# Optimization experiments

Hardware: AMD Instinct MI355X
Metric: run time of the kernel (lower is better)

Reference implementation:

```python
import jax, jax.numpy as jnp
import numpy as np

B, T, C, H = 4, 1024, 2048, 16
D = C // H  # head dim = 128
ALPHA_Q, BETA_Q = -128, 127


def _quant_params(w):
    # symmetric range per tensor, as in get_symmetric_range/get_tensor_quantization_parameters
    beta = float(np.abs(w).max())
    alpha = -beta
    s = (beta - alpha) / (BETA_Q - ALPHA_Q)
    z = int((beta * ALPHA_Q - alpha * BETA_Q) / (beta - alpha))
    return s, z


def _quantize(w, s, z):
    return np.clip(np.round(w / s + z), ALPHA_Q, BETA_Q).astype(np.int8)


def setup_inputs() -> dict:
    key = jax.random.key(0)
    x = jax.random.normal(key, (B, T, C), dtype=jnp.float32)
    rng = np.random.default_rng(0)
    # fp32 master weights (GPT init scale), then quantize per-tensor symmetric int8
    params = {
        'w_attn': rng.normal(0.0, 0.02, (3 * C, C)).astype(np.float32),
        'b_attn': rng.normal(0.0, 0.02, (3 * C,)).astype(np.float32),
        'w_proj': rng.normal(0.0, 0.02, (C, C)).astype(np.float32),
        'b_proj': rng.normal(0.0, 0.02, (C,)).astype(np.float32),
    }
    out = {'x': x}
    for name, arr in params.items():
        s, z = _quant_params(arr)
        out[name + '_q'] = jnp.asarray(_quantize(arr, s, z))
        out['s_' + name] = jnp.float32(s)
        out['z_' + name] = z  # python int, zero-point constant
    return out


def _dequant(wq, s, z):
    # dequantize_tensor: s * (int8 -> int32 - z) -> float32
    return s * (wq.astype(jnp.int32) - z).astype(jnp.float32)


def reference(x, w_attn_q, s_w_attn, z_w_attn, b_attn_q, s_b_attn, z_b_attn,
              w_proj_q, s_w_proj, z_w_proj, b_proj_q, s_b_proj, z_b_proj):
    wa = _dequant(w_attn_q, s_w_attn, z_w_attn)   # [3C, C]
    ba = _dequant(b_attn_q, s_b_attn, z_b_attn)   # [3C]
    wp = _dequant(w_proj_q, s_w_proj, z_w_proj)   # [C, C]
    bp = _dequant(b_proj_q, s_b_proj, z_b_proj)   # [C]

    qkv = jnp.einsum('btc,oc->bto', x, wa) + ba   # [B,T,3C]
    q, k, v = jnp.split(qkv, 3, axis=-1)
    # [B,T,C] -> [B,H,T,D]
    q = q.reshape(B, T, H, D).transpose(0, 2, 1, 3)
    k = k.reshape(B, T, H, D).transpose(0, 2, 1, 3)
    v = v.reshape(B, T, H, D).transpose(0, 2, 1, 3)

    scale = 1.0 / jnp.sqrt(jnp.float32(D))
    scores = jnp.einsum('bhqd,bhkd->bhqk', q, k) * scale  # [B,H,T,T]
    causal = jnp.tril(jnp.ones((T, T), dtype=bool))
    scores = jnp.where(causal, scores, jnp.finfo(scores.dtype).min)
    att = jax.nn.softmax(scores, axis=-1)
    y = jnp.einsum('bhqk,bhkd->bhqd', att, v)      # [B,H,T,D]
    y = y.transpose(0, 2, 1, 3).reshape(B, T, C)

    return jnp.einsum('btc,oc->bto', y, wp) + bp   # [B,T,C]
```

## Files before the change

### kernel.cpp

```cpp
#include <hip/hip_runtime.h>
#include <stdint.h>
#include <math.h>

typedef unsigned short u16;
typedef __attribute__((ext_vector_type(4))) float f32x4;
typedef __attribute__((ext_vector_type(4))) int i32x4;
typedef __attribute__((ext_vector_type(8))) short bf16x8;

__device__ __forceinline__ u16 f2bf(float f) {
  uint32_t u = __float_as_uint(f);
  u += 0x7FFFu + ((u >> 16) & 1u);
  return (u16)(u >> 16);
}

__device__ __forceinline__ void async16(const void* g, void* l) {
  __builtin_amdgcn_global_load_lds(
      (const __attribute__((address_space(1))) void*)g,
      (__attribute__((address_space(3))) void*)l, 16, 0, 0);
}

__global__ void absmax_x(const float4* __restrict__ x, float* __restrict__ amax_arr, int n4) {
  __shared__ float red[4];
  int i = blockIdx.x * 256 + threadIdx.x;
  float m = 0.f;
  for (; i < n4; i += gridDim.x * 256) {
    float4 v = x[i];
    m = fmaxf(m, fmaxf(fmaxf(fabsf(v.x), fabsf(v.y)), fmaxf(fabsf(v.z), fabsf(v.w))));
  }
#pragma unroll
  for (int s = 1; s < 64; s <<= 1) m = fmaxf(m, __shfl_xor(m, s));
  if ((threadIdx.x & 63) == 0) red[threadIdx.x >> 6] = m;
  __syncthreads();
  if (threadIdx.x == 0)
    amax_arr[blockIdx.x] = fmaxf(fmaxf(red[0], red[1]), fmaxf(red[2], red[3]));
}

__global__ void prep_fused(
    const float4* __restrict__ x, char4* __restrict__ xq,
    const int4* __restrict__ waq, char4* __restrict__ wa8, const int* __restrict__ z_wa,
    const int4* __restrict__ wpq, ushort4* __restrict__ wp_bf,
    const float* __restrict__ s_wp, const int* __restrict__ z_wp,
    const float* __restrict__ amax_arr, float* __restrict__ amax_final) {
  const int bid = blockIdx.x;
  const int tid = threadIdx.x;
  if (bid < 8192) {
    const int lane = tid & 63;
    float m = 0.f;
#pragma unroll
    for (int k = 0; k < 4; ++k) {
      float4 a = ((const float4*)amax_arr)[lane * 4 + k];
      m = fmaxf(m, fmaxf(fmaxf(a.x, a.y), fmaxf(a.z, a.w)));
    }
#pragma unroll
    for (int s = 1; s < 64; s <<= 1) m = fmaxf(m, __shfl_xor(m, s));
    if (bid == 0 && tid == 0) amax_final[0] = m;
    const float inv = 127.0f / m;
    const int i = bid * 256 + tid;
    float4 v = x[i];
    char4 r;
    r.x = (char)__float2int_rn(v.x * inv);
    r.y = (char)__float2int_rn(v.y * inv);
    r.z = (char)__float2int_rn(v.z * inv);
    r.w = (char)__float2int_rn(v.w * inv);
    xq[i] = r;
  } else if (bid < 20480) {
    const int zv = z_wa[0];
    const int i = (bid - 8192) * 256 + tid;
    int4 v = waq[i];
    char4 r;
    r.x = (char)(v.x - zv); r.y = (char)(v.y - zv);
    r.z = (char)(v.z - zv); r.w = (char)(v.w - zv);
    wa8[i] = r;
  } else {
    const float sv = s_wp[0];
    const int zv = z_wp[0];
    const int i = (bid - 20480) * 256 + tid;
    int4 v = wpq[i];
    ushort4 r;
    r.x = f2bf(sv * (float)(v.x - zv));
    r.y = f2bf(sv * (float)(v.y - zv));
    r.z = f2bf(sv * (float)(v.z - zv));
    r.w = f2bf(sv * (float)(v.w - zv));
    wp_bf[i] = r;
  }
}

__global__ __launch_bounds__(256, 2) void gemm_i8_qkv(
    const char* __restrict__ A, const char* __restrict__ B, int K,
    const float* __restrict__ sw, const float* __restrict__ amaxf,
    const int* __restrict__ bq, const float* __restrict__ bs, const int* __restrict__ bz,
    u16* __restrict__ qb, u16* __restrict__ kb, u16* __restrict__ vT) {
  __shared__ uint8_t sA[16384];
  __shared__ uint8_t sB[16384];
  const int tid = threadIdx.x;
  const int wave = tid >> 6, lane = tid & 63;
  const int quad = lane >> 4, l16 = lane & 15;
  const int wm = wave >> 1, wn = wave & 1;
  const int Mb = blockIdx.y << 7, Nb = blockIdx.x << 7;

  const char* ag[4];
  const char* bg[4];
  int lo[4];
#pragma unroll
  for (int i = 0; i < 4; ++i) {
    int row = wave * 32 + i * 8 + (lane >> 3);
    int c = (lane & 7) ^ (row & 7);
    ag[i] = A + (size_t)(Mb + row) * K + c * 16;
    bg[i] = B + (size_t)(Nb + row) * K + c * 16;
    lo[i] = wave * 4096 + i * 1024 + lane * 16;
  }

  i32x4 acc[4][4] = {};

  for (int kk = 0; kk < K; kk += 128) {
    __syncthreads();
#pragma unroll
    for (int i = 0; i < 4; ++i) {
      async16(ag[i] + kk, sA + lo[i]);
      async16(bg[i] + kk, sB + lo[i]);
    }
    __syncthreads();
#pragma unroll
    for (int ks = 0; ks < 2; ++ks) {
      i32x4 af[4], bfr[4];
#pragma unroll
      for (int t = 0; t < 4; ++t) {
        int m = wm * 64 + t * 16 + l16;
        af[t] = *(const i32x4*)(sA + m * 128 + ((((ks << 2) + quad) ^ (m & 7)) << 4));
        int n = wn * 64 + t * 16 + l16;
        bfr[t] = *(const i32x4*)(sB + n * 128 + ((((ks << 2) + quad) ^ (n & 7)) << 4));
      }
#pragma unroll
      for (int mt = 0; mt < 4; ++mt)
#pragma unroll
        for (int nt = 0; nt < 4; ++nt)
          acc[mt][nt] = __builtin_amdgcn_mfma_i32_16x16x64_i8(af[mt], bfr[nt], acc[mt][nt], 0, 0, 0);
    }
  }

  const float sv = sw[0] * (amaxf[0] / 127.0f);
  const float sbv = bs[0];
  const int zbv = bz[0];
#pragma unroll
  for (int nt = 0; nt < 4; ++nt) {
    const int o = Nb + wn * 64 + nt * 16 + l16;
    const float bias = sbv * (float)(bq[o] - zbv);
    const int which = o >> 11;
    const int cc = o & 2047;
    const int h = cc >> 7, d = cc & 127;
#pragma unroll
    for (int mt = 0; mt < 4; ++mt) {
      const int m0 = Mb + wm * 64 + mt * 16 + quad * 4;
      const int bi = m0 >> 10, t0 = m0 & 1023;
      const size_t bhx = (size_t)bi * 16 + h;
      if (which == 2) {
        ushort4 pv;
        pv.x = f2bf((float)acc[mt][nt][0] * sv + bias);
        pv.y = f2bf((float)acc[mt][nt][1] * sv + bias);
        pv.z = f2bf((float)acc[mt][nt][2] * sv + bias);
        pv.w = f2bf((float)acc[mt][nt][3] * sv + bias);
        *(ushort4*)(vT + (bhx * 128 + d) * 1024 + t0) = pv;
      } else {
        u16* dst = (which == 0 ? qb : kb) + (bhx * 1024 + t0) * 128 + d;
#pragma unroll
        for (int r = 0; r < 4; ++r) dst[r * 128] = f2bf((float)acc[mt][nt][r] * sv + bias);
      }
    }
  }
}

__global__ __launch_bounds__(256, 2) void gemm_bt_out(
    const u16* __restrict__ A, const u16* __restrict__ B, int K, int N,
    const int* __restrict__ bq, const float* __restrict__ bs, const int* __restrict__ bz,
    float* __restrict__ out) {
  __shared__ uint8_t sA[16384];
  __shared__ uint8_t sB[16384];
  const int tid = threadIdx.x;
  const int wave = tid >> 6, lane = tid & 63;
  const int quad = lane >> 4, l16 = lane & 15;
  const int wm = wave >> 1, wn = wave & 1;
  const int Mb = blockIdx.y << 7, Nb = blockIdx.x << 7;

  const u16* ag[4];
  const u16* bg[4];
  int lo[4];
#pragma unroll
  for (int i = 0; i < 4; ++i) {
    int row = wave * 32 + i * 8 + (lane >> 3);
    int c = (lane & 7) ^ (row & 7);
    ag[i] = A + (size_t)(Mb + row) * K + c * 8;
    bg[i] = B + (size_t)(Nb + row) * K + c * 8;
    lo[i] = wave * 4096 + i * 1024 + lane * 16;
  }

  f32x4 acc[4][4] = {};

  for (int kk = 0; kk < K; kk += 64) {
    __syncthreads();
#pragma unroll
    for (int i = 0; i < 4; ++i) {
      async16(ag[i] + kk, sA + lo[i]);
      async16(bg[i] + kk, sB + lo[i]);
    }
    __syncthreads();
#pragma unroll
    for (int ks = 0; ks < 2; ++ks) {
      bf16x8 af[4], bfr[4];
#pragma unroll
      for (int t = 0; t < 4; ++t) {
        int m = wm * 64 + t * 16 + l16;
        af[t] = *(const bf16x8*)(sA + m * 128 + ((((ks << 2) + quad) ^ (m & 7)) << 4));
        int n = wn * 64 + t * 16 + l16;
        bfr[t] = *(const bf16x8*)(sB + n * 128 + ((((ks << 2) + quad) ^ (n & 7)) << 4));
      }
#pragma unroll
      for (int mt = 0; mt < 4; ++mt)
#pragma unroll
        for (int nt = 0; nt < 4; ++nt)
          acc[mt][nt] = __builtin_amdgcn_mfma_f32_16x16x32_bf16(af[mt], bfr[nt], acc[mt][nt], 0, 0, 0);
    }
  }

  const float sbv = bs[0];
  const int zbv = bz[0];
#pragma unroll
  for (int nt = 0; nt < 4; ++nt) {
    const int o = Nb + wn * 64 + nt * 16 + l16;
    const float bias = sbv * (float)(bq[o] - zbv);
#pragma unroll
    for (int mt = 0; mt < 4; ++mt) {
      const int m0 = Mb + wm * 64 + mt * 16 + quad * 4;
#pragma unroll
      for (int r = 0; r < 4; ++r)
        out[(size_t)(m0 + r) * N + o] = acc[mt][nt][r] + bias;
    }
  }
}

__global__ __launch_bounds__(256, 2) void attn_fwd(
    const u16* __restrict__ qg, const u16* __restrict__ kg,
    const u16* __restrict__ vg, u16* __restrict__ yb) {
  __shared__ uint8_t smem[81920];
  uint8_t* sVb = smem + 32768;
  uint8_t* sP = smem + 65536;
  const int tid = threadIdx.x;
  const int wave = tid >> 6, lane = tid & 63;
  const int quad = lane >> 4, l16 = lane & 15;
  const int bh = blockIdx.x;
  const int y = blockIdx.y;
  const int qi = (y < 4) ? (7 - y) : (y - 4);
  const int qbase = qi << 7;
  const size_t base = (size_t)bh << 17;
  const u16* Q = qg + base;
  const u16* Kp = kg + base;
  const u16* Vp = vg + base;

#pragma unroll
  for (int i = 0; i < 8; ++i) {
    int off = wave * 8192 + i * 1024;
    int row = (off >> 8) + quad;
    int c = l16 ^ (row & 15);
    async16(Q + (size_t)(qbase + row) * 128 + c * 8, smem + off + lane * 16);
  }
  __syncthreads();
  bf16x8 qf[2][4];
#pragma unroll
  for (int mi = 0; mi < 2; ++mi)
#pragma unroll
    for (int ks = 0; ks < 4; ++ks) {
      int m = wave * 32 + mi * 16 + l16;
      qf[mi][ks] = *(const bf16x8*)(smem + m * 256 + ((((ks << 2) + quad) ^ (m & 15)) << 4));
    }
  asm volatile("s_waitcnt lgkmcnt(0)" ::: "memory");
  __builtin_amdgcn_sched_barrier(0);
  __builtin_amdgcn_s_barrier();

#define STAGEKV(TB, SL) do {                                                  \
    _Pragma("unroll")                                                         \
    for (int i_ = 0; i_ < 4; ++i_) {                                          \
      int off_ = wave * 4096 + i_ * 1024;                                     \
      int rowk_ = (off_ >> 8) + quad;                                         \
      int ck_ = l16 ^ (rowk_ & 15);                                           \
      async16(Kp + (size_t)((TB) + rowk_) * 128 + ck_ * 8,                    \
              smem + (SL) * 16384 + off_ + lane * 16);                        \
      int rowd_ = (off_ >> 7) + (lane >> 3);                                  \
      int cv_ = (lane & 7) ^ (rowd_ & 7);                                     \
      async16(Vp + (size_t)rowd_ * 1024 + (TB) + cv_ * 8,                     \
              sVb + (SL) * 16384 + off_ + lane * 16);                         \
    }                                                                         \
  } while (0)

  f32x4 accO[2][8] = {};
  float lacc[2][4] = {};

  const float scale = 0.088388347648318447f;
  const int jmax = 2 * qi + 1;

  STAGEKV(0, 0);

  for (int j = 0; j <= jmax; ++j) {
    const int tb = j << 6;
    const int jn = (j + 1 <= jmax) ? j + 1 : jmax;
    STAGEKV(jn << 6, (j + 1) & 1);
    asm volatile("s_waitcnt vmcnt(8)" ::: "memory");
    __builtin_amdgcn_s_barrier();
    const uint8_t* sK = smem + (j & 1) * 16384;
    const uint8_t* sV = sVb + (j & 1) * 16384;

    f32x4 sc[2][4] = {};
#pragma unroll
    for (int ks = 0; ks < 4; ++ks) {
      bf16x8 kf[4];
#pragma unroll
      for (int ni = 0; ni < 4; ++ni) {
        int n = ni * 16 + l16;
        kf[ni] = *(const bf16x8*)(sK + n * 256 + ((((ks << 2) + quad) ^ (n & 15)) << 4));
      }
#pragma unroll
      for (int mi = 0; mi < 2; ++mi)
#pragma unroll
        for (int ni = 0; ni < 4; ++ni)
          sc[mi][ni] = __builtin_amdgcn_mfma_f32_16x16x32_bf16(qf[mi][ks], kf[ni], sc[mi][ni], 0, 0, 0);
    }

    const bool needmask = (tb + 63) > qbase;
#pragma unroll
    for (int mi = 0; mi < 2; ++mi) {
      const int row0 = qbase + wave * 32 + mi * 16 + quad * 4;
#pragma unroll
      for (int ni = 0; ni < 4; ++ni) {
        const int col = tb + ni * 16 + l16;
#pragma unroll
        for (int r = 0; r < 4; ++r) {
          float s = sc[mi][ni][r] * scale;
          if (needmask && col > row0 + r) s = -INFINITY;
          float p = __expf(s);
          sc[mi][ni][r] = p;
          lacc[mi][r] += p;
        }
      }
    }

#pragma unroll
    for (int mi = 0; mi < 2; ++mi)
#pragma unroll
      for (int ni = 0; ni < 4; ++ni)
#pragma unroll
        for (int r = 0; r < 4; ++r) {
          int qr = wave * 32 + mi * 16 + quad * 4 + r;
          int kc = ni * 16 + l16;
          *(u16*)(sP + qr * 128 + (((kc >> 3) ^ (qr & 7)) << 4) + (kc & 7) * 2) =
              f2bf(sc[mi][ni][r]);
        }

#pragma unroll
    for (int ks = 0; ks < 2; ++ks) {
      bf16x8 pf[2], vf[8];
#pragma unroll
      for (int mi = 0; mi < 2; ++mi) {
        int m = wave * 32 + mi * 16 + l16;
        pf[mi] = *(const bf16x8*)(sP + m * 128 + ((((ks << 2) + quad) ^ (m & 7)) << 4));
      }
#pragma unroll
      for (int ni = 0; ni < 8; ++ni) {
        int n = ni * 16 + l16;
        vf[ni] = *(const bf16x8*)(sV + n * 128 + ((((ks << 2) + quad) ^ (n & 7)) << 4));
      }
#pragma unroll
      for (int mi = 0; mi < 2; ++mi)
#pragma unroll
        for (int ni = 0; ni < 8; ++ni)
          accO[mi][ni] = __builtin_amdgcn_mfma_f32_16x16x32_bf16(pf[mi], vf[ni], accO[mi][ni], 0, 0, 0);
    }
    __builtin_amdgcn_s_barrier();
  }
  asm volatile("s_waitcnt vmcnt(0)" ::: "memory");

  const int b = bh >> 4, h = bh & 15;
#pragma unroll
  for (int mi = 0; mi < 2; ++mi) {
    float inv[4];
#pragma unroll
    for (int r = 0; r < 4; ++r) {
      float l = lacc[mi][r];
#pragma unroll
      for (int x = 1; x < 16; x <<= 1) l += __shfl_xor(l, x);
      inv[r] = 1.0f / l;
    }
#pragma unroll
    for (int ni = 0; ni < 8; ++ni)
#pragma unroll
      for (int r = 0; r < 4; ++r) {
        int row = qbase + wave * 32 + mi * 16 + quad * 4 + r;
        int col = (h << 7) + ni * 16 + l16;
        yb[((size_t)(b * 1024 + row) << 11) + col] = f2bf(accO[mi][ni][r] * inv[r]);
      }
  }
#undef STAGEKV
}

extern "C" void kernel_launch(void* const* d_in, const int* in_sizes, int n_in,
                              void* d_out, int out_size, void* d_ws, size_t ws_size,
                              hipStream_t stream) {
  const float* x = (const float*)d_in[0];
  const int* waq = (const int*)d_in[1];
  const float* s_wa = (const float*)d_in[2];
  const int* z_wa = (const int*)d_in[3];
  const int* baq = (const int*)d_in[4];
  const float* s_ba = (const float*)d_in[5];
  const int* z_ba = (const int*)d_in[6];
  const int* wpq = (const int*)d_in[7];
  const float* s_wp = (const float*)d_in[8];
  const int* z_wp = (const int*)d_in[9];
  const int* bpq = (const int*)d_in[10];
  const float* s_bp = (const float*)d_in[11];
  const int* z_bp = (const int*)d_in[12];

  char* ws = (char*)d_ws;
  char* xq    = ws + 0;
  char* wa8   = ws + 8388608;
  u16* wp_bf  = (u16*)(ws + 20971520);
  u16* qb     = (u16*)(ws + 29360128);
  u16* kb     = (u16*)(ws + 46137344);
  u16* vT     = (u16*)(ws + 62914560);
  u16* yb     = (u16*)(ws + 79691776);
  float* amax_arr   = (float*)(ws + 96468992);
  float* amax_final = (float*)(ws + 96473088);

  absmax_x<<<1024, 256, 0, stream>>>((const float4*)x, amax_arr, 2097152);
  prep_fused<<<24576, 256, 0, stream>>>(
      (const float4*)x, (char4*)xq,
      (const int4*)waq, (char4*)wa8, z_wa,
      (const int4*)wpq, (ushort4*)wp_bf, s_wp, z_wp,
      amax_arr, amax_final);

  gemm_i8_qkv<<<dim3(48, 32), 256, 0, stream>>>(xq, wa8, 2048, s_wa, amax_final,
                                                baq, s_ba, z_ba, qb, kb, vT);

  attn_fwd<<<dim3(64, 8), 256, 0, stream>>>(qb, kb, vT, yb);

  gemm_bt_out<<<dim3(16, 32), 256, 0, stream>>>(yb, wp_bf, 2048, 2048,
                                                bpq, s_bp, z_bp, (float*)d_out);
}
```

Before: 289.6 us.

## Merge all stages into one persistent kernel with software grid barriers

```diff
diff --git a/kernel.cpp b/kernel.cpp
--- a/kernel.cpp
+++ b/kernel.cpp
@@ -19,261 +19,215 @@
       (__attribute__((address_space(3))) void*)l, 16, 0, 0);
 }
 
-__global__ void absmax_x(const float4* __restrict__ x, float* __restrict__ amax_arr, int n4) {
-  __shared__ float red[4];
-  int i = blockIdx.x * 256 + threadIdx.x;
-  float m = 0.f;
-  for (; i < n4; i += gridDim.x * 256) {
-    float4 v = x[i];
-    m = fmaxf(m, fmaxf(fmaxf(fabsf(v.x), fabsf(v.y)), fmaxf(fabsf(v.z), fabsf(v.w))));
-  }
-#pragma unroll
-  for (int s = 1; s < 64; s <<= 1) m = fmaxf(m, __shfl_xor(m, s));
-  if ((threadIdx.x & 63) == 0) red[threadIdx.x >> 6] = m;
+__device__ __forceinline__ void gbar(unsigned* cnt, unsigned* gen) {
   __syncthreads();
-  if (threadIdx.x == 0)
-    amax_arr[blockIdx.x] = fmaxf(fmaxf(red[0], red[1]), fmaxf(red[2], red[3]));
+  if (threadIdx.x == 0) {
+    unsigned g = __hip_atomic_load(gen, __ATOMIC_RELAXED, __HIP_MEMORY_SCOPE_AGENT);
+    unsigned prev = __hip_atomic_fetch_add(cnt, 1u, __ATOMIC_ACQ_REL, __HIP_MEMORY_SCOPE_AGENT);
+    if (prev == 511u) {
+      __hip_atomic_store(cnt, 0u, __ATOMIC_RELAXED, __HIP_MEMORY_SCOPE_AGENT);
+      __hip_atomic_store(gen, (g + 1u) & 3u, __ATOMIC_RELEASE, __HIP_MEMORY_SCOPE_AGENT);
+    } else {
+      unsigned t = 0;
+      while (__hip_atomic_load(gen, __ATOMIC_RELAXED, __HIP_MEMORY_SCOPE_AGENT) == g) {
+        __builtin_amdgcn_s_sleep(4);
+        if (++t > 2000000u) break;
+      }
+      __builtin_amdgcn_fence(__ATOMIC_ACQUIRE, "agent");
+    }
+  }
+  __syncthreads();
 }
 
-__global__ void prep_fused(
-    const float4* __restrict__ x, char4* __restrict__ xq,
-    const int4* __restrict__ waq, char4* __restrict__ wa8, const int* __restrict__ z_wa,
-    const int4* __restrict__ wpq, ushort4* __restrict__ wp_bf,
-    const float* __restrict__ s_wp, const int* __restrict__ z_wp,
-    const float* __restrict__ amax_arr, float* __restrict__ amax_final) {
-  const int bid = blockIdx.x;
-  const int tid = threadIdx.x;
-  if (bid < 8192) {
-    const int lane = tid & 63;
-    float m = 0.f;
-#pragma unroll
-    for (int k = 0; k < 4; ++k) {
-      float4 a = ((const float4*)amax_arr)[lane * 4 + k];
-      m = fmaxf(m, fmaxf(fmaxf(a.x, a.y), fmaxf(a.z, a.w)));
-    }
-#pragma unroll
-    for (int s = 1; s < 64; s <<= 1) m = fmaxf(m, __shfl_xor(m, s));
-    if (bid == 0 && tid == 0) amax_final[0] = m;
-    const float inv = 127.0f / m;
-    const int i = bid * 256 + tid;
-    float4 v = x[i];
-    char4 r;
-    r.x = (char)__float2int_rn(v.x * inv);
-    r.y = (char)__float2int_rn(v.y * inv);
-    r.z = (char)__float2int_rn(v.z * inv);
-    r.w = (char)__float2int_rn(v.w * inv);
-    xq[i] = r;
-  } else if (bid < 20480) {
-    const int zv = z_wa[0];
-    const int i = (bid - 8192) * 256 + tid;
-    int4 v = waq[i];
-    char4 r;
-    r.x = (char)(v.x - zv); r.y = (char)(v.y - zv);
-    r.z = (char)(v.z - zv); r.w = (char)(v.w - zv);
-    wa8[i] = r;
-  } else {
-    const float sv = s_wp[0];
-    const int zv = z_wp[0];
-    const int i = (bid - 20480) * 256 + tid;
-    int4 v = wpq[i];
-    ushort4 r;
-    r.x = f2bf(sv * (float)(v.x - zv));
-    r.y = f2bf(sv * (float)(v.y - zv));
-    r.z = f2bf(sv * (float)(v.z - zv));
-    r.w = f2bf(sv * (float)(v.w - zv));
-    wp_bf[i] = r;
-  }
-}
-
-__global__ __launch_bounds__(256, 2) void gemm_i8_qkv(
-    const char* __restrict__ A, const char* __restrict__ B, int K,
-    const float* __restrict__ sw, const float* __restrict__ amaxf,
-    const int* __restrict__ bq, const float* __restrict__ bs, const int* __restrict__ bz,
-    u16* __restrict__ qb, u16* __restrict__ kb, u16* __restrict__ vT) {
-  __shared__ uint8_t sA[16384];
-  __shared__ uint8_t sB[16384];
+__global__ __launch_bounds__(256, 2) void mega(
+    const float4* __restrict__ x,
+    const int4* __restrict__ waq, const int* __restrict__ z_wa,
+    const float* __restrict__ s_wa,
+    const int* __restrict__ baq, const float* __restrict__ s_ba, const int* __restrict__ z_ba,
+    const int4* __restrict__ wpq, const float* __restrict__ s_wp, const int* __restrict__ z_wp,
+    const int* __restrict__ bpq, const float* __restrict__ s_bp, const int* __restrict__ z_bp,
+    char* __restrict__ xq, char* __restrict__ wa8, u16* __restrict__ wp_bf,
+    u16* __restrict__ qb, u16* __restrict__ kb, u16* __restrict__ vT,
+    u16* __restrict__ yb, float* __restrict__ partial,
+    unsigned* __restrict__ bcnt, unsigned* __restrict__ bgen,
+    float* __restrict__ out) {
+  __shared__ uint8_t smem[81920];
+  const int rb = blockIdx.x;
   const int tid = threadIdx.x;
   const int wave = tid >> 6, lane = tid & 63;
   const int quad = lane >> 4, l16 = lane & 15;
-  const int wm = wave >> 1, wn = wave & 1;
-  const int Mb = blockIdx.y << 7, Nb = blockIdx.x << 7;
-
-  const char* ag[4];
-  const char* bg[4];
-  int lo[4];
-#pragma unroll
-  for (int i = 0; i < 4; ++i) {
-    int row = wave * 32 + i * 8 + (lane >> 3);
-    int c = (lane & 7) ^ (row & 7);
-    ag[i] = A + (size_t)(Mb + row) * K + c * 16;
-    bg[i] = B + (size_t)(Nb + row) * K + c * 16;
-    lo[i] = wave * 4096 + i * 1024 + lane * 16;
-  }
-
-  i32x4 acc[4][4] = {};
-
-  for (int kk = 0; kk < K; kk += 128) {
+
+  {
+    float m = 0.f;
+    for (int i = rb * 256 + tid; i < 2097152; i += 131072) {
+      float4 v = x[i];
+      m = fmaxf(m, fmaxf(fmaxf(fabsf(v.x), fabsf(v.y)), fmaxf(fabsf(v.z), fabsf(v.w))));
+    }
+#pragma unroll
+    for (int s = 1; s < 64; s <<= 1) m = fmaxf(m, __shfl_xor(m, s));
+    float* red = (float*)smem;
+    if (lane == 0) red[wave] = m;
     __syncthreads();
-#pragma unroll
-    for (int i = 0; i < 4; ++i) {
-      async16(ag[i] + kk, sA + lo[i]);
-      async16(bg[i] + kk, sB + lo[i]);
+    if (tid == 0)
+      partial[rb] = fmaxf(fmaxf(red[0], red[1]), fmaxf(red[2], red[3]));
+  }
+  gbar(bcnt, bgen);
+
+  float amax_val;
+  {
+    float m = 0.f;
+#pragma unroll
+    for (int k = 0; k < 2; ++k) {
+      float4 a = ((const float4*)partial)[lane * 2 + k];
+      m = fmaxf(m, fmaxf(fmaxf(a.x, a.y), fmaxf(a.z, a.w)));
+    }
+#pragma unroll
+    for (int s = 1; s < 64; s <<= 1) m = fmaxf(m, __shfl_xor(m, s));
+    amax_val = m;
+    const float inv = 127.0f / m;
+    for (int i = rb * 256 + tid; i < 2097152; i += 131072) {
+      float4 v = x[i];
+      char4 r;
+      r.x = (char)__float2int_rn(v.x * inv);
+      r.y = (char)__float2int_rn(v.y * inv);
+      r.z = (char)__float2int_rn(v.z * inv);
+      r.w = (char)__float2int_rn(v.w * inv);
+      ((char4*)xq)[i] = r;
+    }
+    const int zv = z_wa[0];
+    for (int i = rb * 256 + tid; i < 3145728; i += 131072) {
+      int4 v = waq[i];
+      char4 r;
+      r.x = (char)(v.x - zv); r.y = (char)(v.y - zv);
+      r.z = (char)(v.z - zv); r.w = (char)(v.w - zv);
+      ((char4*)wa8)[i] = r;
+    }
+    const float svp = s_wp[0];
+    const int zvp = z_wp[0];
+    for (int i = rb * 256 + tid; i < 1048576; i += 131072) {
+      int4 v = wpq[i];
+      ushort4 r;
+      r.x = f2bf(svp * (float)(v.x - zvp));
+      r.y = f2bf(svp * (float)(v.y - zvp));
+      r.z = f2bf(svp * (float)(v.z - zvp));
+      r.w = f2bf(svp * (float)(v.w - zvp));
+      ((ushort4*)wp_bf)[i] = r;
+    }
+  }
+  gbar(bcnt, bgen);
+
+  {
+    uint8_t* sA = smem;
+    uint8_t* sB = smem + 16384;
+    const char* A = xq;
+    const char* B = wa8;
+    const int wm = wave >> 1, wn = wave & 1;
+    const float sv = s_wa[0] * (amax_val / 127.0f);
+    const float sbv = s_ba[0];
+    const int zbv = z_ba[0];
+#pragma unroll 1
+    for (int vt = 0; vt < 3; ++vt) {
+      const int vb = rb + (vt << 9);
+      const int Mb = (vb / 48) << 7, Nb = (vb % 48) << 7;
+      const char* ag[4];
+      const char* bg[4];
+      int lo[4];
+#pragma unroll
+      for (int i = 0; i < 4; ++i) {
+        int row = wave * 32 + i * 8 + (lane >> 3);
+        int c = (lane & 7) ^ (row & 7);
+        ag[i] = A + (size_t)(Mb + row) * 2048 + c * 16;
+        bg[i] = B + (size_t)(Nb + row) * 2048 + c * 16;
+        lo[i] = wave * 4096 + i * 1024 + lane * 16;
+      }
+      i32x4 acc[4][4] = {};
+#pragma unroll 1
+      for (int kk = 0; kk < 2048; kk += 128) {
+        __syncthreads();
+#pragma unroll
+        for (int i = 0; i < 4; ++i) {
+          async16(ag[i] + kk, sA + lo[i]);
+          async16(bg[i] + kk, sB + lo[i]);
+        }
+        __syncthreads();
+#pragma unroll
+        for (int ks = 0; ks < 2; ++ks) {
+          i32x4 af[4], bfr[4];
+#pragma unroll
+          for (int t = 0; t < 4; ++t) {
+            int m = wm * 64 + t * 16 + l16;
+            af[t] = *(const i32x4*)(sA + m * 128 + ((((ks << 2) + quad) ^ (m & 7)) << 4));
+            int n = wn * 64 + t * 16 + l16;
+            bfr[t] = *(const i32x4*)(sB + n * 128 + ((((ks << 2) + quad) ^ (n & 7)) << 4));
+          }
+#pragma unroll
+          for (int mt = 0; mt < 4; ++mt)
+#pragma unroll
+            for (int nt = 0; nt < 4; ++nt)
+              acc[mt][nt] = __builtin_amdgcn_mfma_i32_16x16x64_i8(af[mt], bfr[nt], acc[mt][nt], 0, 0, 0);
+        }
+      }
+#pragma unroll
+      for (int nt = 0; nt < 4; ++nt) {
+        const int o = Nb + wn * 64 + nt * 16 + l16;
+        const float bias = sbv * (float)(baq[o] - zbv);
+        const int which = o >> 11;
+        const int cc = o & 2047;
+        const int h = cc >> 7, d = cc & 127;
+#pragma unroll
+        for (int mt = 0; mt < 4; ++mt) {
+          const int m0 = Mb + wm * 64 + mt * 16 + quad * 4;
+          const int bi = m0 >> 10, t0 = m0 & 1023;
+          const size_t bhx = (size_t)bi * 16 + h;
+          if (which == 2) {
+            ushort4 pv;
+            pv.x = f2bf((float)acc[mt][nt][0] * sv + bias);
+            pv.y = f2bf((float)acc[mt][nt][1] * sv + bias);
+            pv.z = f2bf((float)acc[mt][nt][2] * sv + bias);
+            pv.w = f2bf((float)acc[mt][nt][3] * sv + bias);
+            *(ushort4*)(vT + (bhx * 128 + d) * 1024 + t0) = pv;
+          } else {
+            u16* dst = (which == 0 ? qb : kb) + (bhx * 1024 + t0) * 128 + d;
+#pragma unroll
+            for (int r = 0; r < 4; ++r) dst[r * 128] = f2bf((float)acc[mt][nt][r] * sv + bias);
+          }
+        }
+      }
+    }
+  }
+  gbar(bcnt, bgen);
+
+  {
+    uint8_t* sVb = smem + 32768;
+    uint8_t* sP = smem + 65536;
+    const int bh = rb & 63;
+    const int y = rb >> 6;
+    const int qi = (y < 4) ? (7 - y) : (y - 4);
+    const int qbase = qi << 7;
+    const size_t base = (size_t)bh << 17;
+    const u16* Q = qb + base;
+    const u16* Kp = kb + base;
+    const u16* Vp = vT + base;
+
+#pragma unroll
+    for (int i = 0; i < 8; ++i) {
+      int off = wave * 8192 + i * 1024;
+      int row = (off >> 8) + quad;
+      int c = l16 ^ (row & 15);
+      async16(Q + (size_t)(qbase + row) * 128 + c * 8, smem + off + lane * 16);
     }
     __syncthreads();
-#pragma unroll
-    for (int ks = 0; ks < 2; ++ks) {
-      i32x4 af[4], bfr[4];
-#pragma unroll
-      for (int t = 0; t < 4; ++t) {
-        int m = wm * 64 + t * 16 + l16;
-        af[t] = *(const i32x4*)(sA + m * 128 + ((((ks << 2) + quad) ^ (m & 7)) << 4));
-        int n = wn * 64 + t * 16 + l16;
-        bfr[t] = *(const i32x4*)(sB + n * 128 + ((((ks << 2) + quad) ^ (n & 7)) << 4));
-      }
-#pragma unroll
-      for (int mt = 0; mt < 4; ++mt)
-#pragma unroll
-        for (int nt = 0; nt < 4; ++nt)
-          acc[mt][nt] = __builtin_amdgcn_mfma_i32_16x16x64_i8(af[mt], bfr[nt], acc[mt][nt], 0, 0, 0);
-    }
-  }
-
-  const float sv = sw[0] * (amaxf[0] / 127.0f);
-  const float sbv = bs[0];
-  const int zbv = bz[0];
-#pragma unroll
-  for (int nt = 0; nt < 4; ++nt) {
-    const int o = Nb + wn * 64 + nt * 16 + l16;
-    const float bias = sbv * (float)(bq[o] - zbv);
-    const int which = o >> 11;
-    const int cc = o & 2047;
-    const int h = cc >> 7, d = cc & 127;
-#pragma unroll
-    for (int mt = 0; mt < 4; ++mt) {
-      const int m0 = Mb + wm * 64 + mt * 16 + quad * 4;
-      const int bi = m0 >> 10, t0 = m0 & 1023;
-      const size_t bhx = (size_t)bi * 16 + h;
-      if (which == 2) {
-        ushort4 pv;
-        pv.x = f2bf((float)acc[mt][nt][0] * sv + bias);
-        pv.y = f2bf((float)acc[mt][nt][1] * sv + bias);
-        pv.z = f2bf((float)acc[mt][nt][2] * sv + bias);
-        pv.w = f2bf((float)acc[mt][nt][3] * sv + bias);
-        *(ushort4*)(vT + (bhx * 128 + d) * 1024 + t0) = pv;
-      } else {
-        u16* dst = (which == 0 ? qb : kb) + (bhx * 1024 + t0) * 128 + d;
-#pragma unroll
-        for (int r = 0; r < 4; ++r) dst[r * 128] = f2bf((float)acc[mt][nt][r] * sv + bias);
-      }
-    }
-  }
-}
-
-__global__ __launch_bounds__(256, 2) void gemm_bt_out(
-    const u16* __restrict__ A, const u16* __restrict__ B, int K, int N,
-    const int* __restrict__ bq, const float* __restrict__ bs, const int* __restrict__ bz,
-    float* __restrict__ out) {
-  __shared__ uint8_t sA[16384];
-  __shared__ uint8_t sB[16384];
-  const int tid = threadIdx.x;
-  const int wave = tid >> 6, lane = tid & 63;
-  const int quad = lane >> 4, l16 = lane & 15;
-  const int wm = wave >> 1, wn = wave & 1;
-  const int Mb = blockIdx.y << 7, Nb = blockIdx.x << 7;
-
-  const u16* ag[4];
-  const u16* bg[4];
-  int lo[4];
-#pragma unroll
-  for (int i = 0; i < 4; ++i) {
-    int row = wave * 32 + i * 8 + (lane >> 3);
-    int c = (lane & 7) ^ (row & 7);
-    ag[i] = A + (size_t)(Mb + row) * K + c * 8;
-    bg[i] = B + (size_t)(Nb + row) * K + c * 8;
-    lo[i] = wave * 4096 + i * 1024 + lane * 16;
-  }
-
-  f32x4 acc[4][4] = {};
-
-  for (int kk = 0; kk < K; kk += 64) {
-    __syncthreads();
-#pragma unroll
-    for (int i = 0; i < 4; ++i) {
-      async16(ag[i] + kk, sA + lo[i]);
-      async16(bg[i] + kk, sB + lo[i]);
-    }
-    __syncthreads();
-#pragma unroll
-    for (int ks = 0; ks < 2; ++ks) {
-      bf16x8 af[4], bfr[4];
-#pragma unroll
-      for (int t = 0; t < 4; ++t) {
-        int m = wm * 64 + t * 16 + l16;
-        af[t] = *(const bf16x8*)(sA + m * 128 + ((((ks << 2) + quad) ^ (m & 7)) << 4));
-        int n = wn * 64 + t * 16 + l16;
-        bfr[t] = *(const bf16x8*)(sB + n * 128 + ((((ks << 2) + quad) ^ (n & 7)) << 4));
-      }
-#pragma unroll
-      for (int mt = 0; mt < 4; ++mt)
-#pragma unroll
-        for (int nt = 0; nt < 4; ++nt)
-          acc[mt][nt] = __builtin_amdgcn_mfma_f32_16x16x32_bf16(af[mt], bfr[nt], acc[mt][nt], 0, 0, 0);
-    }
-  }
-
-  const float sbv = bs[0];
-  const int zbv = bz[0];
-#pragma unroll
-  for (int nt = 0; nt < 4; ++nt) {
-    const int o = Nb + wn * 64 + nt * 16 + l16;
-    const float bias = sbv * (float)(bq[o] - zbv);
-#pragma unroll
-    for (int mt = 0; mt < 4; ++mt) {
-      const int m0 = Mb + wm * 64 + mt * 16 + quad * 4;
-#pragma unroll
-      for (int r = 0; r < 4; ++r)
-        out[(size_t)(m0 + r) * N + o] = acc[mt][nt][r] + bias;
-    }
-  }
-}
-
-__global__ __launch_bounds__(256, 2) void attn_fwd(
-    const u16* __restrict__ qg, const u16* __restrict__ kg,
-    const u16* __restrict__ vg, u16* __restrict__ yb) {
-  __shared__ uint8_t smem[81920];
-  uint8_t* sVb = smem + 32768;
-  uint8_t* sP = smem + 65536;
-  const int tid = threadIdx.x;
-  const int wave = tid >> 6, lane = tid & 63;
-  const int quad = lane >> 4, l16 = lane & 15;
-  const int bh = blockIdx.x;
-  const int y = blockIdx.y;
-  const int qi = (y < 4) ? (7 - y) : (y - 4);
-  const int qbase = qi << 7;
-  const size_t base = (size_t)bh << 17;
-  const u16* Q = qg + base;
-  const u16* Kp = kg + base;
-  const u16* Vp = vg + base;
-
-#pragma unroll
-  for (int i = 0; i < 8; ++i) {
-    int off = wave * 8192 + i * 1024;
-    int row = (off >> 8) + quad;
-    int c = l16 ^ (row & 15);
-    async16(Q + (size_t)(qbase + row) * 128 + c * 8, smem + off + lane * 16);
-  }
-  __syncthreads();
-  bf16x8 qf[2][4];
-#pragma unroll
-  for (int mi = 0; mi < 2; ++mi)
-#pragma unroll
-    for (int ks = 0; ks < 4; ++ks) {
-      int m = wave * 32 + mi * 16 + l16;
-      qf[mi][ks] = *(const bf16x8*)(smem + m * 256 + ((((ks << 2) + quad) ^ (m & 15)) << 4));
-    }
-  asm volatile("s_waitcnt lgkmcnt(0)" ::: "memory");
-  __builtin_amdgcn_sched_barrier(0);
-  __builtin_amdgcn_s_barrier();
+    bf16x8 qf[2][4];
+#pragma unroll
+    for (int mi = 0; mi < 2; ++mi)
+#pragma unroll
+      for (int ks = 0; ks < 4; ++ks) {
+        int m = wave * 32 + mi * 16 + l16;
+        qf[mi][ks] = *(const bf16x8*)(smem + m * 256 + ((((ks << 2) + quad) ^ (m & 15)) << 4));
+      }
+    asm volatile("s_waitcnt lgkmcnt(0)" ::: "memory");
+    __builtin_amdgcn_sched_barrier(0);
+    __builtin_amdgcn_s_barrier();
 
 #define STAGEKV(TB, SL) do {                                                  \
     _Pragma("unroll")                                                         \
@@ -290,126 +244,191 @@
     }                                                                         \
   } while (0)
 
-  f32x4 accO[2][8] = {};
-  float lacc[2][4] = {};
-
-  const float scale = 0.088388347648318447f;
-  const int jmax = 2 * qi + 1;
-
-  STAGEKV(0, 0);
-
-  for (int j = 0; j <= jmax; ++j) {
-    const int tb = j << 6;
-    const int jn = (j + 1 <= jmax) ? j + 1 : jmax;
-    STAGEKV(jn << 6, (j + 1) & 1);
-    asm volatile("s_waitcnt vmcnt(8)" ::: "memory");
-    __builtin_amdgcn_s_barrier();
-    const uint8_t* sK = smem + (j & 1) * 16384;
-    const uint8_t* sV = sVb + (j & 1) * 16384;
-
-    f32x4 sc[2][4] = {};
-#pragma unroll
-    for (int ks = 0; ks < 4; ++ks) {
-      bf16x8 kf[4];
-#pragma unroll
-      for (int ni = 0; ni < 4; ++ni) {
-        int n = ni * 16 + l16;
-        kf[ni] = *(const bf16x8*)(sK + n * 256 + ((((ks << 2) + quad) ^ (n & 15)) << 4));
-      }
+    f32x4 accO[2][8] = {};
+    float lacc[2][4] = {};
+    const float scale = 0.088388347648318447f;
+    const int jmax = 2 * qi + 1;
+
+    STAGEKV(0, 0);
+
+    for (int j = 0; j <= jmax; ++j) {
+      const int tb = j << 6;
+      const int jn = (j + 1 <= jmax) ? j + 1 : jmax;
+      STAGEKV(jn << 6, (j + 1) & 1);
+      asm volatile("s_waitcnt vmcnt(8)" ::: "memory");
+      __builtin_amdgcn_s_barrier();
+      const uint8_t* sK = smem + (j & 1) * 16384;
+      const uint8_t* sV = sVb + (j & 1) * 16384;
+
+      f32x4 sc[2][4] = {};
+#pragma unroll
+      for (int ks = 0; ks < 4; ++ks) {
+        bf16x8 kf[4];
+#pragma unroll
+        for (int ni = 0; ni < 4; ++ni) {
+          int n = ni * 16 + l16;
+          kf[ni] = *(const bf16x8*)(sK + n * 256 + ((((ks << 2) + quad) ^ (n & 15)) << 4));
+        }
+#pragma unroll
+        for (int mi = 0; mi < 2; ++mi)
+#pragma unroll
+          for (int ni = 0; ni < 4; ++ni)
+            sc[mi][ni] = __builtin_amdgcn_mfma_f32_16x16x32_bf16(qf[mi][ks], kf[ni], sc[mi][ni], 0, 0, 0);
+      }
+
+      const bool needmask = (tb + 63) > qbase;
+#pragma unroll
+      for (int mi = 0; mi < 2; ++mi) {
+        const int row0 = qbase + wave * 32 + mi * 16 + quad * 4;
+#pragma unroll
+        for (int ni = 0; ni < 4; ++ni) {
+          const int col = tb + ni * 16 + l16;
+#pragma unroll
+          for (int r = 0; r < 4; ++r) {
+            float s = sc[mi][ni][r] * scale;
+            if (needmask && col > row0 + r) s = -INFINITY;
+            float p = __expf(s);
+            sc[mi][ni][r] = p;
+            lacc[mi][r] += p;
+          }
+        }
+      }
+
 #pragma unroll
       for (int mi = 0; mi < 2; ++mi)
 #pragma unroll
         for (int ni = 0; ni < 4; ++ni)
-          sc[mi][ni] = __builtin_amdgcn_mfma_f32_16x16x32_bf16(qf[mi][ks], kf[ni], sc[mi][ni], 0, 0, 0);
-    }
-
-    const bool needmask = (tb + 63) > qbase;
+#pragma unroll
+          for (int r = 0; r < 4; ++r) {
+            int qr = wave * 32 + mi * 16 + quad * 4 + r;
+            int kc = ni * 16 + l16;
+            *(u16*)(sP + qr * 128 + (((kc >> 3) ^ (qr & 7)) << 4) + (kc & 7) * 2) =
+                f2bf(sc[mi][ni][r]);
+          }
+
+#pragma unroll
+      for (int ks = 0; ks < 2; ++ks) {
+        bf16x8 pf[2], vf[8];
+#pragma unroll
+        for (int mi = 0; mi < 2; ++mi) {
+          int m = wave * 32 + mi * 16 + l16;
+          pf[mi] = *(const bf16x8*)(sP + m * 128 + ((((ks << 2) + quad) ^ (m & 7)) << 4));
+        }
+#pragma unroll
+        for (int ni = 0; ni < 8; ++ni) {
+          int n = ni * 16 + l16;
+          vf[ni] = *(const bf16x8*)(sV + n * 128 + ((((ks << 2) + quad) ^ (n & 7)) << 4));
+        }
+#pragma unroll
+        for (int mi = 0; mi < 2; ++mi)
+#pragma unroll
+          for (int ni = 0; ni < 8; ++ni)
+            accO[mi][ni] = __builtin_amdgcn_mfma_f32_16x16x32_bf16(pf[mi], vf[ni], accO[mi][ni], 0, 0, 0);
+      }
+      __builtin_amdgcn_s_barrier();
+    }
+    asm volatile("s_waitcnt vmcnt(0)" ::: "memory");
+
+    const int b = bh >> 4, h = bh & 15;
 #pragma unroll
     for (int mi = 0; mi < 2; ++mi) {
-      const int row0 = qbase + wave * 32 + mi * 16 + quad * 4;
-#pragma unroll
-      for (int ni = 0; ni < 4; ++ni) {
-        const int col = tb + ni * 16 + l16;
+      float inv[4];
+#pragma unroll
+      for (int r = 0; r < 4; ++r) {
+        float l = lacc[mi][r];
+#pragma unroll
+        for (int xw = 1; xw < 16; xw <<= 1) l += __shfl_xor(l, xw);
+        inv[r] = 1.0f / l;
+      }
+#pragma unroll
+      for (int ni = 0; ni < 8; ++ni)
 #pragma unroll
         for (int r = 0; r < 4; ++r) {
-          float s = sc[mi][ni][r] * scale;
-          if (needmask && col > row0 + r) s = -INFINITY;
-          float p = __expf(s);
-          sc[mi][ni][r] = p;
-          lacc[mi][r] += p;
-        }
-      }
-    }
-
-#pragma unroll
-    for (int mi = 0; mi < 2; ++mi)
-#pragma unroll
-      for (int ni = 0; ni < 4; ++ni)
-#pragma unroll
-        for (int r = 0; r < 4; ++r) {
-          int qr = wave * 32 + mi * 16 + quad * 4 + r;
-          int kc = ni * 16 + l16;
-          *(u16*)(sP + qr * 128 + (((kc >> 3) ^ (qr & 7)) << 4) + (kc & 7) * 2) =
-              f2bf(sc[mi][ni][r]);
-        }
-
-#pragma unroll
-    for (int ks = 0; ks < 2; ++ks) {
-      bf16x8 pf[2], vf[8];
-#pragma unroll
-      for (int mi = 0; mi < 2; ++mi) {
-        int m = wave * 32 + mi * 16 + l16;
-        pf[mi] = *(const bf16x8*)(sP + m * 128 + ((((ks << 2) + quad) ^ (m & 7)) << 4));
-      }
-#pragma unroll
-      for (int ni = 0; ni < 8; ++ni) {
-        int n = ni * 16 + l16;
-        vf[ni] = *(const bf16x8*)(sV + n * 128 + ((((ks << 2) + quad) ^ (n & 7)) << 4));
-      }
-#pragma unroll
-      for (int mi = 0; mi < 2; ++mi)
-#pragma unroll
-        for (int ni = 0; ni < 8; ++ni)
-          accO[mi][ni] = __builtin_amdgcn_mfma_f32_16x16x32_bf16(pf[mi], vf[ni], accO[mi][ni], 0, 0, 0);
-    }
-    __builtin_amdgcn_s_barrier();
-  }
-  asm volatile("s_waitcnt vmcnt(0)" ::: "memory");
-
-  const int b = bh >> 4, h = bh & 15;
-#pragma unroll
-  for (int mi = 0; mi < 2; ++mi) {
-    float inv[4];
-#pragma unroll
-    for (int r = 0; r < 4; ++r) {
-      float l = lacc[mi][r];
-#pragma unroll
-      for (int x = 1; x < 16; x <<= 1) l += __shfl_xor(l, x);
-      inv[r] = 1.0f / l;
-    }
-#pragma unroll
-    for (int ni = 0; ni < 8; ++ni)
-#pragma unroll
-      for (int r = 0; r < 4; ++r) {
-        int row = qbase + wave * 32 + mi * 16 + quad * 4 + r;
-        int col = (h << 7) + ni * 16 + l16;
-        yb[((size_t)(b * 1024 + row) << 11) + col] = f2bf(accO[mi][ni][r] * inv[r]);
-      }
-  }
+          int row = qbase + wave * 32 + mi * 16 + quad * 4 + r;
+          int col = (h << 7) + ni * 16 + l16;
+          yb[((size_t)(b * 1024 + row) << 11) + col] = f2bf(accO[mi][ni][r] * inv[r]);
+        }
+    }
 #undef STAGEKV
+  }
+  gbar(bcnt, bgen);
+
+  {
+    uint8_t* sA = smem;
+    uint8_t* sB = smem + 16384;
+    const u16* A = yb;
+    const u16* B = wp_bf;
+    const int wm = wave >> 1, wn = wave & 1;
+    const int Mb = (rb >> 4) << 7, Nb = (rb & 15) << 7;
+
+    const u16* ag[4];
+    const u16* bg[4];
+    int lo[4];
+#pragma unroll
+    for (int i = 0; i < 4; ++i) {
+      int row = wave * 32 + i * 8 + (lane >> 3);
+      int c = (lane & 7) ^ (row & 7);
+      ag[i] = A + (size_t)(Mb + row) * 2048 + c * 8;
+      bg[i] = B + (size_t)(Nb + row) * 2048 + c * 8;
+      lo[i] = wave * 4096 + i * 1024 + lane * 16;
+    }
+
+    f32x4 acc[4][4] = {};
+#pragma unroll 1
+    for (int kk = 0; kk < 2048; kk += 64) {
+      __syncthreads();
+#pragma unroll
+      for (int i = 0; i < 4; ++i) {
+        async16(ag[i] + kk, sA + lo[i]);
+        async16(bg[i] + kk, sB + lo[i]);
+      }
+      __syncthreads();
+#pragma unroll
+      for (int ks = 0; ks < 2; ++ks) {
+        bf16x8 af[4], bfr[4];
+#pragma unroll
+        for (int t = 0; t < 4; ++t) {
+          int m = wm * 64 + t * 16 + l16;
+          af[t] = *(const bf16x8*)(sA + m * 128 + ((((ks << 2) + quad) ^ (m & 7)) << 4));
+          int n = wn * 64 + t * 16 + l16;
+          bfr[t] = *(const bf16x8*)(sB + n * 128 + ((((ks << 2) + quad) ^ (n & 7)) << 4));
+        }
+#pragma unroll
+        for (int mt = 0; mt < 4; ++mt)
+#pragma unroll
+          for (int nt = 0; nt < 4; ++nt)
+            acc[mt][nt] = __builtin_amdgcn_mfma_f32_16x16x32_bf16(af[mt], bfr[nt], acc[mt][nt], 0, 0, 0);
+      }
+    }
+
+    const float sbv = s_bp[0];
+    const int zbv = z_bp[0];
+#pragma unroll
+    for (int nt = 0; nt < 4; ++nt) {
+      const int o = Nb + wn * 64 + nt * 16 + l16;
+      const float bias = sbv * (float)(bpq[o] - zbv);
+#pragma unroll
+      for (int mt = 0; mt < 4; ++mt) {
+        const int m0 = Mb + wm * 64 + mt * 16 + quad * 4;
+#pragma unroll
+        for (int r = 0; r < 4; ++r)
+          out[(size_t)(m0 + r) * 2048 + o] = acc[mt][nt][r] + bias;
+      }
+    }
+  }
 }
 
 extern "C" void kernel_launch(void* const* d_in, const int* in_sizes, int n_in,
                               void* d_out, int out_size, void* d_ws, size_t ws_size,
                               hipStream_t stream) {
-  const float* x = (const float*)d_in[0];
-  const int* waq = (const int*)d_in[1];
+  const float4* x = (const float4*)d_in[0];
+  const int4* waq = (const int4*)d_in[1];
   const float* s_wa = (const float*)d_in[2];
   const int* z_wa = (const int*)d_in[3];
   const int* baq = (const int*)d_in[4];
   const float* s_ba = (const float*)d_in[5];
   const int* z_ba = (const int*)d_in[6];
-  const int* wpq = (const int*)d_in[7];
+  const int4* wpq = (const int4*)d_in[7];
   const float* s_wp = (const float*)d_in[8];
   const int* z_wp = (const int*)d_in[9];
   const int* bpq = (const int*)d_in[10];
@@ -424,21 +443,15 @@
   u16* kb     = (u16*)(ws + 46137344);
   u16* vT     = (u16*)(ws + 62914560);
   u16* yb     = (u16*)(ws + 79691776);
-  float* amax_arr   = (float*)(ws + 96468992);
-  float* amax_final = (float*)(ws + 96473088);
-
-  absmax_x<<<1024, 256, 0, stream>>>((const float4*)x, amax_arr, 2097152);
-  prep_fused<<<24576, 256, 0, stream>>>(
-      (const float4*)x, (char4*)xq,
-      (const int4*)waq, (char4*)wa8, z_wa,
-      (const int4*)wpq, (ushort4*)wp_bf, s_wp, z_wp,
-      amax_arr, amax_final);
-
-  gemm_i8_qkv<<<dim3(48, 32), 256, 0, stream>>>(xq, wa8, 2048, s_wa, amax_final,
-                                                baq, s_ba, z_ba, qb, kb, vT);
-
-  attn_fwd<<<dim3(64, 8), 256, 0, stream>>>(qb, kb, vT, yb);
-
-  gemm_bt_out<<<dim3(16, 32), 256, 0, stream>>>(yb, wp_bf, 2048, 2048,
-                                                bpq, s_bp, z_bp, (float*)d_out);
+  float* partial = (float*)(ws + 96468992);
+  unsigned* bcnt = (unsigned*)(ws + 96471040);
+  unsigned* bgen = (unsigned*)(ws + 96471044);
+
+  hipMemsetAsync(bcnt, 0, 8, stream);
+
+  mega<<<512, 256, 0, stream>>>(
+      x, waq, z_wa, s_wa, baq, s_ba, z_ba, wpq, s_wp, z_wp,
+      bpq, s_bp, z_bp,
+      xq, wa8, wp_bf, qb, kb, vT, yb, partial, bcnt, bgen,
+      (float*)d_out);
 }
```

Measured after the change: 489.3 us. +69.0%, slower.
